# Performance work log

Measured on AMD Instinct MI355X. Metric: run time of the kernel, lower is better.

Reference implementation:

```python
import jax, jax.numpy as jnp
import numpy as np

D_MODEL = 1024


def setup_inputs() -> dict:
    key = jax.random.key(0)
    ks = jax.random.split(key, 9)
    B, S, D = 4, 2048, D_MODEL
    scale = 1.0 / np.sqrt(D)
    inp = {
        "tokens": jax.random.normal(ks[0], (B, S, D), dtype=jnp.float32),
        "Wq": jax.random.normal(ks[1], (D, D), dtype=jnp.float32) * scale,
        "bq": jnp.zeros((D,), dtype=jnp.float32),
        "Wk": jax.random.normal(ks[2], (D, D), dtype=jnp.float32) * scale,
        "bk": jnp.zeros((D,), dtype=jnp.float32),
        "Wv": jax.random.normal(ks[3], (D, D), dtype=jnp.float32) * scale,
        "bv": jnp.zeros((D,), dtype=jnp.float32),
        "Wo": jax.random.normal(ks[4], (D, D), dtype=jnp.float32) * scale,
        "bo": jnp.zeros((D,), dtype=jnp.float32),
    }
    return inp


def reference(tokens, Wq, bq, Wk, bk, Wv, bv, Wo, bo):
    # use_activation=True, use_residual=True
    residual = tokens
    x = jax.nn.gelu(tokens, approximate=False)  # F.gelu default is exact (erf)
    q = jnp.einsum("bsd,de->bse", x, Wq) + bq
    k = jnp.einsum("bsd,de->bse", x, Wk) + bk
    v = jnp.einsum("bsd,de->bse", x, Wv) + bv
    scale = 1.0 / jnp.sqrt(jnp.asarray(tokens.shape[-1], dtype=tokens.dtype))
    scores = jnp.einsum("bqd,bkd->bqk", q, k) * scale  # [B,S,S]
    attn = jax.nn.softmax(scores, axis=-1)
    mixed = jnp.einsum("bqk,bkd->bqd", attn, v)
    out = jnp.einsum("bsd,de->bse", mixed, Wo) + bo
    return out + residual
```

## Files before the change

### kernel.cpp

```cpp
#include <hip/hip_runtime.h>
#include <hip/hip_bf16.h>
#include <cstdint>
#include <cstddef>

typedef unsigned short u16;
using frag_ab = __attribute__((ext_vector_type(8))) short;
using f32x4   = __attribute__((ext_vector_type(4))) float;

__device__ __forceinline__ u16 f2bf(float x) {
    __hip_bfloat16 h = __float2bfloat16(x);
    return *reinterpret_cast<u16*>(&h);
}

__device__ __forceinline__ void gload_lds16(const u16* g, u16* l) {
    __builtin_amdgcn_global_load_lds(
        (const __attribute__((address_space(1))) uint32_t*)g,
        (__attribute__((address_space(3)))       uint32_t*)l,
        16, 0, 0);
}

#define WAITV4() do { asm volatile("s_waitcnt vmcnt(4)" ::: "memory"); \
                      __builtin_amdgcn_sched_barrier(0); } while (0)
#define WAITV0() do { asm volatile("s_waitcnt vmcnt(0)" ::: "memory"); \
                      __builtin_amdgcn_sched_barrier(0); } while (0)
#define BAR()    do { asm volatile("" ::: "memory"); __builtin_amdgcn_s_barrier(); \
                      __builtin_amdgcn_sched_barrier(0); } while (0)
#define LGKMC(N) do { asm volatile("s_waitcnt lgkmcnt(" #N ")" ::: "memory"); \
                      __builtin_amdgcn_sched_barrier(0); } while (0)
#define LGKM0()  LGKMC(0)

template<int EPI, int BN_>
__global__ __launch_bounds__(512, 2)
void gemm8p(const u16* __restrict__ A, const u16* __restrict__ Bt,
            void* __restrict__ C0,
            const float* __restrict__ b0, const float* __restrict__ resid,
            int K, int lda, int ldb, int ldc,
            long long sA, long long sB, long long sC, float alpha,
            float* __restrict__ partials)
{
    constexpr int NFQ    = BN_ / 64;
    constexpr int WN     = BN_ / 2;
    constexpr int BUFSTR = 16384 + BN_ * 64;
    __shared__ __align__(16) u16 lds[2 * BUFSTR];

    const int z = blockIdx.z;
    A  += (long long)z * sA;
    Bt += (long long)z * sB;

    const int gx  = gridDim.x;
    const int nwg = gx * gridDim.y;
    const int cpx = nwg >> 3;
    int lin = blockIdx.x + gx * blockIdx.y;
    lin = (lin & 7) * cpx + (lin >> 3);
    const int m0 = (lin / gx) * 256;
    const int n0 = (lin % gx) * BN_;

    const int t    = threadIdx.x;
    const int lane = t & 63;
    const int wave = t >> 6;
    const int wm   = wave >> 1;
    const int wn   = wave & 1;

    const int r0  = t >> 3;
    const int ssw = (t & 7) ^ (r0 & 7);
    const u16* gsA0_0 = A  + (size_t)(m0 +       r0) * lda + ssw * 8;
    const u16* gsA0_1 = A  + (size_t)(m0 +  64 + r0) * lda + ssw * 8;
    const u16* gsA1_0 = A  + (size_t)(m0 + 128 + r0) * lda + ssw * 8;
    const u16* gsA1_1 = A  + (size_t)(m0 + 192 + r0) * lda + ssw * 8;
    const u16* gsB0_0 = Bt + (size_t)(n0 +       r0) * ldb + ssw * 8;
    const u16* gsB0_1 = Bt + (size_t)(n0 +  64 + r0) * ldb + ssw * 8;
    const u16* gsB1_0 = (BN_ == 256) ? Bt + (size_t)(n0 + 128 + r0) * ldb + ssw * 8 : gsB0_0;
    const u16* gsB1_1 = (BN_ == 256) ? Bt + (size_t)(n0 + 192 + r0) * ldb + ssw * 8 : gsB0_1;

#define OPO_A 0
#define OPO_B 16384
#define STAGE(BI, OP, H, KT) do {                                              \
    gload_lds16(gs##OP##H##_0 + (size_t)(KT) * 64,                             \
                lds + (BI) * BUFSTR + OPO_##OP + (H) * 8192 + t * 8);          \
    gload_lds16(gs##OP##H##_1 + (size_t)(KT) * 64,                             \
                lds + (BI) * BUFSTR + OPO_##OP + (H) * 8192 + 4096 + t * 8);   \
} while (0)

    const int ar   = lane & 15;
    const int ko   = lane >> 4;
    const int aoff = (wm * 64 + ar) * 64;
    const int boff = OPO_B + (wn * WN + ar) * 64;
    const int as0  = ((0 + ko) ^ (ar & 7)) * 8;
    const int as1  = ((4 + ko) ^ (ar & 7)) * 8;

    frag_ab areg[2][2];
    frag_ab breg[2][NFQ][2];
    f32x4   acc[4][2 * NFQ] = {};

#define RDA(BI, MQ) do { _Pragma("unroll") for (int mf = 0; mf < 2; ++mf) {    \
    areg[mf][0] = *(const frag_ab*)(lds + (BI)*BUFSTR + aoff + ((MQ)*2+mf)*1024 + as0); \
    areg[mf][1] = *(const frag_ab*)(lds + (BI)*BUFSTR + aoff + ((MQ)*2+mf)*1024 + as1); } } while (0)

#define RDB(BI, NQ) do { _Pragma("unroll") for (int jf = 0; jf < NFQ; ++jf) {  \
    breg[NQ][jf][0] = *(const frag_ab*)(lds + (BI)*BUFSTR + boff + ((NQ)*NFQ+jf)*1024 + as0); \
    breg[NQ][jf][1] = *(const frag_ab*)(lds + (BI)*BUFSTR + boff + ((NQ)*NFQ+jf)*1024 + as1); } } while (0)

#define MMAQ(MQ, NQ) do { __builtin_amdgcn_s_setprio(1);                       \
    _Pragma("unroll") for (int mf = 0; mf < 2; ++mf)                           \
    _Pragma("unroll") for (int jf = 0; jf < NFQ; ++jf) {                       \
        acc[(MQ)*2+mf][(NQ)*NFQ+jf] = __builtin_amdgcn_mfma_f32_16x16x32_bf16( \
            areg[mf][0], breg[NQ][jf][0], acc[(MQ)*2+mf][(NQ)*NFQ+jf], 0,0,0); \
        acc[(MQ)*2+mf][(NQ)*NFQ+jf] = __builtin_amdgcn_mfma_f32_16x16x32_bf16( \
            areg[mf][1], breg[NQ][jf][1], acc[(MQ)*2+mf][(NQ)*NFQ+jf], 0,0,0); \
    } __builtin_amdgcn_s_setprio(0); } while (0)

    const int nk = K / 64;
    STAGE(0, A, 0, 0); STAGE(0, A, 1, 0); STAGE(0, B, 0, 0);
    if constexpr (BN_ == 256) STAGE(0, B, 1, 0);
    STAGE(1, B, 0, 1); STAGE(1, A, 0, 1);
    WAITV4();
    BAR();

    const int nIter = nk >> 1;
    for (int it = 0; it < nIter; ++it) {
        const int O  = 2 * it + 1;
        const int E2 = (2 * it + 2 < nk) ? 2 * it + 2 : nk - 1;
        const int O2 = (2 * it + 3 < nk) ? 2 * it + 3 : nk - 1;

        RDA(0, 0); RDB(0, 0);
        STAGE(1, A, 1, O);
        if constexpr (BN_ == 256) LGKMC(8);
        BAR(); LGKM0(); MMAQ(0, 0);
        RDB(0, 1);
        if constexpr (BN_ == 256) STAGE(1, B, 1, O);
        BAR(); LGKM0(); MMAQ(0, 1);
        RDA(0, 1);
        STAGE(0, B, 0, E2);
        BAR(); LGKM0(); MMAQ(1, 0);
        STAGE(0, A, 0, E2);
        WAITV4();
        BAR(); MMAQ(1, 1);
        RDA(1, 0); RDB(1, 0);
        STAGE(0, A, 1, E2);
        if constexpr (BN_ == 256) LGKMC(8);
        BAR(); LGKM0(); MMAQ(0, 0);
        RDB(1, 1);
        if constexpr (BN_ == 256) STAGE(0, B, 1, E2);
        BAR(); LGKM0(); MMAQ(0, 1);
        RDA(1, 1);
        STAGE(1, B, 0, O2);
        BAR(); LGKM0(); MMAQ(1, 0);
        STAGE(1, A, 0, O2);
        WAITV4();
        BAR(); MMAQ(1, 1);
    }

    const int cr = (lane >> 4) * 4;
    const int cc = lane & 15;

    float* fl = (float*)lds;
    if constexpr (EPI == 2) {
        WAITV0();
        BAR();
        if (t < 256) {
            const float* p = partials + ((size_t)z * 2048 + m0 + t) * 16;
            float s = 0.0f;
            #pragma unroll
            for (int i = 0; i < 16; ++i) s += p[i];
            fl[t] = 1.0f / s;
        }
        BAR();
    }

    float rs[4][4];
    if constexpr (EPI == 1) {
        #pragma unroll
        for (int mi = 0; mi < 4; ++mi)
            #pragma unroll
            for (int r = 0; r < 4; ++r) rs[mi][r] = 0.0f;
    }

    #pragma unroll
    for (int mi = 0; mi < 4; ++mi) {
        const int rowb = m0 + wm * 64 + mi * 16 + cr;
        const int rloc = wm * 64 + mi * 16 + cr;
        #pragma unroll
        for (int gj = 0; gj < 2 * NFQ; ++gj) {
            const int col = n0 + wn * WN + gj * 16 + cc;
            const float bvv = (EPI == 3) ? b0[col] : 0.0f;
            #pragma unroll
            for (int r = 0; r < 4; ++r) {
                const size_t row = (size_t)(rowb + r);
                float v = acc[mi][gj][r];
                if (EPI == 1) { v = __expf(v * alpha); rs[mi][r] += v; }
                if (EPI == 2) v *= fl[rloc + r];
                v += bvv;
                if (EPI == 3) {
                    v += resid[row * ldc + col];
                    ((float*)C0)[(size_t)z * sC + row * ldc + col] = v;
                } else {
                    ((u16*)C0)[(size_t)z * sC + row * ldc + col] = f2bf(v);
                }
            }
        }
    }

    if constexpr (EPI == 1) {
        #pragma unroll
        for (int mi = 0; mi < 4; ++mi)
            #pragma unroll
            for (int r = 0; r < 4; ++r) {
                float s = rs[mi][r];
                s += __shfl_xor(s, 1); s += __shfl_xor(s, 2);
                s += __shfl_xor(s, 4); s += __shfl_xor(s, 8);
                rs[mi][r] = s;
            }
        if (cc == 0) {
            const int chunk = (n0 >> 7) + wn;
            #pragma unroll
            for (int mi = 0; mi < 4; ++mi) {
                const int rowb = m0 + wm * 64 + mi * 16 + cr;
                #pragma unroll
                for (int r = 0; r < 4; ++r)
                    partials[((size_t)z * 2048 + rowb + r) * 16 + chunk] = rs[mi][r];
            }
        }
    }
#undef STAGE
#undef RDA
#undef RDB
#undef MMAQ
#undef OPO_A
#undef OPO_B
}

__global__ __launch_bounds__(256, 2)
void gemm128_qkv(const u16* __restrict__ A, const u16* __restrict__ Bt,
                 void* __restrict__ C0, void* __restrict__ C1, void* __restrict__ C2,
                 const float* __restrict__ b0, const float* __restrict__ b1,
                 const float* __restrict__ b2,
                 int K, int lda, int ldb, int ldc)
{
    constexpr int BUFSTR = 16384;
    __shared__ __align__(16) u16 lds[2 * BUFSTR];

    const int gx  = gridDim.x;
    const int nwg = gx * gridDim.y;
    const int cpx = nwg >> 3;
    int lin = blockIdx.x + gx * blockIdx.y;
    lin = (lin & 7) * cpx + (lin >> 3);
    const int m0 = (lin / gx) * 128;
    const int n0 = (lin % gx) * 128;

    const int t    = threadIdx.x;
    const int lane = t & 63;
    const int wave = t >> 6;
    const int wm   = wave >> 1;
    const int wn   = wave & 1;

    const int r0  = t >> 3;
    const int ssw = (t & 7) ^ (r0 & 7);
    const u16* gsA0_0 = A  + (size_t)(m0 +       r0) * lda + ssw * 8;
    const u16* gsA0_1 = A  + (size_t)(m0 +  32 + r0) * lda + ssw * 8;
    const u16* gsA1_0 = A  + (size_t)(m0 +  64 + r0) * lda + ssw * 8;
    const u16* gsA1_1 = A  + (size_t)(m0 +  96 + r0) * lda + ssw * 8;
    const u16* gsB0_0 = Bt + (size_t)(n0 +       r0) * ldb + ssw * 8;
    const u16* gsB0_1 = Bt + (size_t)(n0 +  32 + r0) * ldb + ssw * 8;
    const u16* gsB1_0 = Bt + (size_t)(n0 +  64 + r0) * ldb + ssw * 8;
    const u16* gsB1_1 = Bt + (size_t)(n0 +  96 + r0) * ldb + ssw * 8;

#define OPO_A 0
#define OPO_B 8192
#define STAGE(BI, OP, H, KT) do {                                              \
    gload_lds16(gs##OP##H##_0 + (size_t)(KT) * 64,                             \
                lds + (BI) * BUFSTR + OPO_##OP + (H) * 4096 + t * 8);          \
    gload_lds16(gs##OP##H##_1 + (size_t)(KT) * 64,                             \
                lds + (BI) * BUFSTR + OPO_##OP + (H) * 4096 + 2048 + t * 8);   \
} while (0)

    const int ar   = lane & 15;
    const int ko   = lane >> 4;
    const int aoff = (wm * 64 + ar) * 64;
    const int boff = OPO_B + (wn * 64 + ar) * 64;
    const int as0  = ((0 + ko) ^ (ar & 7)) * 8;
    const int as1  = ((4 + ko) ^ (ar & 7)) * 8;

    frag_ab areg[2][2];
    frag_ab breg[2][2][2];
    f32x4   acc[4][4] = {};

#define RDA(BI, MQ) do { _Pragma("unroll") for (int mf = 0; mf < 2; ++mf) {    \
    areg[mf][0] = *(const frag_ab*)(lds + (BI)*BUFSTR + aoff + ((MQ)*2+mf)*1024 + as0); \
    areg[mf][1] = *(const frag_ab*)(lds + (BI)*BUFSTR + aoff + ((MQ)*2+mf)*1024 + as1); } } while (0)

#define RDB(BI, NQ) do { _Pragma("unroll") for (int jf = 0; jf < 2; ++jf) {    \
    breg[NQ][jf][0] = *(const frag_ab*)(lds + (BI)*BUFSTR + boff + ((NQ)*2+jf)*1024 + as0); \
    breg[NQ][jf][1] = *(const frag_ab*)(lds + (BI)*BUFSTR + boff + ((NQ)*2+jf)*1024 + as1); } } while (0)

#define MMAQ(MQ, NQ) do { __builtin_amdgcn_s_setprio(1);                       \
    _Pragma("unroll") for (int mf = 0; mf < 2; ++mf)                           \
    _Pragma("unroll") for (int jf = 0; jf < 2; ++jf) {                         \
        acc[(MQ)*2+mf][(NQ)*2+jf] = __builtin_amdgcn_mfma_f32_16x16x32_bf16(   \
            areg[mf][0], breg[NQ][jf][0], acc[(MQ)*2+mf][(NQ)*2+jf], 0,0,0);   \
        acc[(MQ)*2+mf][(NQ)*2+jf] = __builtin_amdgcn_mfma_f32_16x16x32_bf16(   \
            areg[mf][1], breg[NQ][jf][1], acc[(MQ)*2+mf][(NQ)*2+jf], 0,0,0);   \
    } __builtin_amdgcn_s_setprio(0); } while (0)

    const int nk = K / 64;
    STAGE(0, A, 0, 0); STAGE(0, A, 1, 0); STAGE(0, B, 0, 0); STAGE(0, B, 1, 0);
    STAGE(1, B, 0, 1); STAGE(1, A, 0, 1);
    WAITV4();
    BAR();

    const int nIter = nk >> 1;
    for (int it = 0; it < nIter; ++it) {
        const int O  = 2 * it + 1;
        const int E2 = (2 * it + 2 < nk) ? 2 * it + 2 : nk - 1;
        const int O2 = (2 * it + 3 < nk) ? 2 * it + 3 : nk - 1;

        RDA(0, 0); RDB(0, 0); STAGE(1, A, 1, O);  BAR(); LGKM0(); MMAQ(0, 0);
        RDB(0, 1);            STAGE(1, B, 1, O);  BAR(); LGKM0(); MMAQ(0, 1);
        RDA(0, 1);            STAGE(0, B, 0, E2); BAR(); LGKM0(); MMAQ(1, 0);
        STAGE(0, A, 0, E2);   WAITV4();           BAR();          MMAQ(1, 1);
        RDA(1, 0); RDB(1, 0); STAGE(0, A, 1, E2); BAR(); LGKM0(); MMAQ(0, 0);
        RDB(1, 1);            STAGE(0, B, 1, E2); BAR(); LGKM0(); MMAQ(0, 1);
        RDA(1, 1);            STAGE(1, B, 0, O2); BAR(); LGKM0(); MMAQ(1, 0);
        STAGE(1, A, 0, O2);   WAITV4();           BAR();          MMAQ(1, 1);
    }

    const int cr = (lane >> 4) * 4;
    const int cc = lane & 15;

    const int plane = n0 >> 10;
    const int nc    = n0 & 1023;

    if (plane == 2) {
        WAITV0();
        BAR();
        constexpr int TP = 136;
        u16* T = lds;
        #pragma unroll
        for (int mi = 0; mi < 4; ++mi) {
            const int rloc = wm * 64 + mi * 16 + cr;
            #pragma unroll
            for (int gj = 0; gj < 4; ++gj) {
                const int cl = wn * 64 + gj * 16 + cc;
                const float bvv = b2[nc + cl];
                #pragma unroll
                for (int r = 0; r < 4; ++r)
                    T[cl * TP + rloc + r] = f2bf(acc[mi][gj][r] + bvv);
            }
        }
        BAR();
        const int bb   = m0 >> 11;
        const int s0   = m0 & 2047;
        const int d    = t >> 1;
        const int half = t & 1;
        const u16* src = T + d * TP + half * 64;
        u16* dg = (u16*)C2 + (size_t)bb * 1024 * 2048
                + (size_t)(nc + d) * 2048 + s0 + half * 64;
        #pragma unroll
        for (int j = 0; j < 8; ++j)
            ((uint4*)dg)[j] = ((const uint4*)src)[j];
    } else {
        void*        Cw = (plane == 0) ? C0 : C1;
        const float* bw = (plane == 0) ? b0 : b1;
        #pragma unroll
        for (int mi = 0; mi < 4; ++mi) {
            const int rowb = m0 + wm * 64 + mi * 16 + cr;
            #pragma unroll
            for (int gj = 0; gj < 4; ++gj) {
                const int col = nc + wn * 64 + gj * 16 + cc;
                const float bvv = bw[col];
                #pragma unroll
                for (int r = 0; r < 4; ++r) {
                    const size_t row = (size_t)(rowb + r);
                    ((u16*)Cw)[row * ldc + col] = f2bf(acc[mi][gj][r] + bvv);
                }
            }
        }
    }
#undef STAGE
#undef RDA
#undef RDB
#undef MMAQ
#undef OPO_A
#undef OPO_B
}

__global__ __launch_bounds__(256)
void prep_kernel(const float4* __restrict__ in, uint2* __restrict__ outp,
                 const float* __restrict__ W0, const float* __restrict__ W1,
                 const float* __restrict__ W2, const float* __restrict__ W3,
                 u16* __restrict__ WT, int D, int NG)
{
    __shared__ float tile[32][33];
    const int b = blockIdx.x;
    const int t = threadIdx.x;
    if (b < NG) {
        const int i = b * 256 + t;
        float4 x = in[i];
        auto g = [](float v) { return 0.5f * v * (1.0f + erff(v * 0.70710678118654752f)); };
        union { u16 u[4]; uint2 q; } pk;
        pk.u[0] = f2bf(g(x.x));
        pk.u[1] = f2bf(g(x.y));
        pk.u[2] = f2bf(g(x.z));
        pk.u[3] = f2bf(g(x.w));
        outp[i] = pk.q;
        return;
    }
    const int j   = b - NG;
    const int z   = j >> 10;
    const int rem = j & 1023;
    const int n0  = (rem & 31) * 32;
    const int k0  = (rem >> 5) * 32;
    const float* W = (z == 0) ? W0 : (z == 1) ? W1 : (z == 2) ? W2 : W3;
    u16* o = WT + (size_t)z * D * D;
    const int tx = t & 31, ty = t >> 5;
    #pragma unroll
    for (int r = 0; r < 4; ++r)
        tile[ty + 8 * r][tx] = W[(size_t)(k0 + ty + 8 * r) * D + n0 + tx];
    __syncthreads();
    #pragma unroll
    for (int r = 0; r < 4; ++r)
        o[(size_t)(n0 + ty + 8 * r) * D + k0 + tx] = f2bf(tile[tx][ty + 8 * r]);
}

extern "C" void kernel_launch(void* const* d_in, const int* in_sizes, int n_in,
                              void* d_out, int out_size, void* d_ws, size_t ws_size,
                              hipStream_t stream)
{
    const int B = 4, S = 2048, D = 1024;
    const int M = B * S;

    const float* tokens = (const float*)d_in[0];
    const float* Wq = (const float*)d_in[1];
    const float* bq = (const float*)d_in[2];
    const float* Wk = (const float*)d_in[3];
    const float* bk = (const float*)d_in[4];
    const float* Wv = (const float*)d_in[5];
    const float* bv = (const float*)d_in[6];
    const float* Wo = (const float*)d_in[7];
    const float* bo = (const float*)d_in[8];
    float* out = (float*)d_out;

    char* ws = (char*)d_ws;
    size_t o = 0;
    u16* x_bf = (u16*)(ws + o); o += (size_t)M * D * 2;
    u16* wT   = (u16*)(ws + o); o += (size_t)4 * D * D * 2;
    u16* q_bf = (u16*)(ws + o); o += (size_t)M * D * 2;
    u16* k_bf = (u16*)(ws + o); o += (size_t)M * D * 2;
    u16* vt   = (u16*)(ws + o); o += (size_t)M * D * 2;
    u16*   E        = (u16*)(ws + o);   o += (size_t)B * S * S * 2;
    float* partials = (float*)(ws + o); o += (size_t)B * S * 16 * 4;
    u16* mixed = x_bf;

    const int NG = M * D / 4 / 256;
    prep_kernel<<<dim3(NG + 4096), dim3(256), 0, stream>>>(
        (const float4*)tokens, (uint2*)x_bf, Wq, Wk, Wv, Wo, wT, D, NG);

    gemm128_qkv<<<dim3(3 * D / 128, M / 128, 1), dim3(256), 0, stream>>>(
        x_bf, wT, q_bf, k_bf, vt, bq, bk, bv, D, D, D, D);

    gemm8p<1, 256><<<dim3(S / 256, S / 256, B), dim3(512), 0, stream>>>(
        q_bf, k_bf, E, nullptr, nullptr,
        D, D, D, S, (long long)S * D, (long long)S * D, (long long)S * S, 0.03125f,
        partials);

    gemm8p<2, 128><<<dim3(D / 128, S / 256, B), dim3(512), 0, stream>>>(
        E, vt, mixed, nullptr, nullptr,
        S, S, S, D, (long long)S * S, (long long)D * S, (long long)S * D, 1.0f,
        partials);

    gemm8p<3, 128><<<dim3(D / 128, M / 256, 1), dim3(512), 0, stream>>>(
        mixed, wT + 3 * D * D, out, bo, tokens,
        D, D, D, D, 0, 0, 0, 1.0f, nullptr);
}
```

Before: 172.7 us.

## Split QKV projection into 256-tile QK GEMM and separate V-transpose GEMM

Replaces the single 128x128-tile fused QKV GEMM with a new 512-thread 256x256-tile kernel for Q and K, using a triple-buffered A / double-buffered B LDS pipeline, plus a dedicated 128-tile kernel for V with its transposed store. The larger tiles raise arithmetic intensity and cut global traffic for the Q/K projection. The V epilogue now packs four bf16 values into one LDS store, and the GELU prep kernel processes eight elements per thread. The cost is an extra kernel launch, a very large LDS footprint and high register pressure in the 256-tile kernel, which may limit occupancy.

```diff
diff --git a/kernel.cpp b/kernel.cpp
--- a/kernel.cpp
+++ b/kernel.cpp
@@ -229,12 +229,139 @@
 #undef OPO_B
 }
 
+__global__ __launch_bounds__(512, 2)
+void gemmQK3(const u16* __restrict__ A, const u16* __restrict__ Bt,
+             u16* __restrict__ C0, const float* __restrict__ b0,
+             const float* __restrict__ b1,
+             int K, int lda, int ldb, int ldc, long long sC)
+{
+    __shared__ __align__(16) u16 lds[81920];
+
+    const int gx  = gridDim.x;
+    const int nwg = gx * gridDim.y;
+    const int cpx = nwg >> 3;
+    int lin = blockIdx.x + gx * blockIdx.y;
+    lin = (lin & 7) * cpx + (lin >> 3);
+    const int m0 = (lin / gx) * 256;
+    const int n0 = (lin % gx) * 256;
+
+    const int t    = threadIdx.x;
+    const int lane = t & 63;
+    const int wave = t >> 6;
+    const int wm   = wave >> 1;
+    const int wn   = wave & 1;
+
+    const int r0  = t >> 3;
+    const int ssw = (t & 7) ^ (r0 & 7);
+    const u16* gsA_0 = A  + (size_t)(m0 +       r0) * lda + ssw * 8;
+    const u16* gsA_1 = A  + (size_t)(m0 +  64 + r0) * lda + ssw * 8;
+    const u16* gsA_2 = A  + (size_t)(m0 + 128 + r0) * lda + ssw * 8;
+    const u16* gsA_3 = A  + (size_t)(m0 + 192 + r0) * lda + ssw * 8;
+    const u16* gsB_0 = Bt + (size_t)(n0 +       r0) * ldb + ssw * 8;
+    const u16* gsB_1 = Bt + (size_t)(n0 +  64 + r0) * ldb + ssw * 8;
+    const u16* gsB_2 = Bt + (size_t)(n0 + 128 + r0) * ldb + ssw * 8;
+    const u16* gsB_3 = Bt + (size_t)(n0 + 192 + r0) * ldb + ssw * 8;
+
+#define STA(BUF, H, KT) do {                                                   \
+    gload_lds16(((H) ? gsA_2 : gsA_0) + (size_t)(KT) * 64,                     \
+                lds + (BUF) * 16384 + (H) * 8192 + t * 8);                     \
+    gload_lds16(((H) ? gsA_3 : gsA_1) + (size_t)(KT) * 64,                     \
+                lds + (BUF) * 16384 + (H) * 8192 + 4096 + t * 8);              \
+} while (0)
+#define STB(BUF, H, KT) do {                                                   \
+    gload_lds16(((H) ? gsB_2 : gsB_0) + (size_t)(KT) * 64,                     \
+                lds + 49152 + (BUF) * 16384 + (H) * 8192 + t * 8);             \
+    gload_lds16(((H) ? gsB_3 : gsB_1) + (size_t)(KT) * 64,                     \
+                lds + 49152 + (BUF) * 16384 + (H) * 8192 + 4096 + t * 8);      \
+} while (0)
+
+    const int ar   = lane & 15;
+    const int ko   = lane >> 4;
+    const int aoff = (wm * 64 + ar) * 64;
+    const int boff = 49152 + (wn * 128 + ar) * 64;
+    const int as0  = ((0 + ko) ^ (ar & 7)) * 8;
+    const int as1  = ((4 + ko) ^ (ar & 7)) * 8;
+
+    frag_ab areg[2][2];
+    frag_ab breg[2][4][2];
+    f32x4   acc[4][8] = {};
+
+#define RDA3(AB, MQ) do { _Pragma("unroll") for (int mf = 0; mf < 2; ++mf) {   \
+    areg[mf][0] = *(const frag_ab*)(lds + (AB) + aoff + ((MQ)*2+mf)*1024 + as0); \
+    areg[mf][1] = *(const frag_ab*)(lds + (AB) + aoff + ((MQ)*2+mf)*1024 + as1); } } while (0)
+
+#define RDB3(BB, NQ) do { _Pragma("unroll") for (int jf = 0; jf < 4; ++jf) {   \
+    breg[NQ][jf][0] = *(const frag_ab*)(lds + (BB) + boff + ((NQ)*4+jf)*1024 + as0); \
+    breg[NQ][jf][1] = *(const frag_ab*)(lds + (BB) + boff + ((NQ)*4+jf)*1024 + as1); } } while (0)
+
+#define MMAQ3(MQ, NQ) do { __builtin_amdgcn_s_setprio(1);                      \
+    _Pragma("unroll") for (int mf = 0; mf < 2; ++mf)                           \
+    _Pragma("unroll") for (int jf = 0; jf < 4; ++jf) {                         \
+        acc[(MQ)*2+mf][(NQ)*4+jf] = __builtin_amdgcn_mfma_f32_16x16x32_bf16(   \
+            areg[mf][0], breg[NQ][jf][0], acc[(MQ)*2+mf][(NQ)*4+jf], 0,0,0);   \
+        acc[(MQ)*2+mf][(NQ)*4+jf] = __builtin_amdgcn_mfma_f32_16x16x32_bf16(   \
+            areg[mf][1], breg[NQ][jf][1], acc[(MQ)*2+mf][(NQ)*4+jf], 0,0,0);   \
+    } __builtin_amdgcn_s_setprio(0); } while (0)
+
+    const int nk = K / 64;
+    STA(0, 0, 0); STA(0, 1, 0);
+    STB(0, 0, 0); STB(0, 1, 0);
+    STA(1, 0, 1); STA(1, 1, 1);
+    WAITV4();
+    BAR();
+
+    int ab = 0, bb = 0;
+    for (int tt = 0; tt < nk; ++tt) {
+        const int ab2 = (ab + 2 >= 3) ? ab - 1 : ab + 2;
+        const int bb1 = bb ^ 1;
+        const int tB  = (tt + 1 < nk) ? tt + 1 : nk - 1;
+        const int tA  = (tt + 2 < nk) ? tt + 2 : nk - 1;
+        const int AB = ab * 16384, BB = bb * 16384;
+        RDA3(AB, 0); RDB3(BB, 0);
+        STB(bb1, 0, tB);
+        LGKMC(8);
+        BAR(); LGKM0(); MMAQ3(0, 0);
+        RDB3(BB, 1);
+        STB(bb1, 1, tB);
+        BAR(); LGKM0(); MMAQ3(0, 1);
+        RDA3(AB, 1);
+        STA(ab2, 0, tA);
+        BAR(); LGKM0(); MMAQ3(1, 0);
+        STA(ab2, 1, tA);
+        WAITV4();
+        BAR(); MMAQ3(1, 1);
+        ab = (ab + 1 >= 3) ? 0 : ab + 1;
+        bb = bb1;
+    }
+
+    const int cr = (lane >> 4) * 4;
+    const int cc = lane & 15;
+    #pragma unroll
+    for (int mi = 0; mi < 4; ++mi) {
+        const int rowb = m0 + wm * 64 + mi * 16 + cr;
+        #pragma unroll
+        for (int gj = 0; gj < 8; ++gj) {
+            const int col = n0 + wn * 128 + gj * 16 + cc;
+            const int plane = col >> 10;
+            const int cl    = col & 1023;
+            const float bvv = ((plane == 0) ? b0 : b1)[cl];
+            u16* Cw = C0 + (size_t)plane * sC;
+            #pragma unroll
+            for (int r = 0; r < 4; ++r)
+                Cw[(size_t)(rowb + r) * ldc + cl] = f2bf(acc[mi][gj][r] + bvv);
+        }
+    }
+#undef STA
+#undef STB
+#undef RDA3
+#undef RDB3
+#undef MMAQ3
+}
+
 __global__ __launch_bounds__(256, 2)
-void gemm128_qkv(const u16* __restrict__ A, const u16* __restrict__ Bt,
-                 void* __restrict__ C0, void* __restrict__ C1, void* __restrict__ C2,
-                 const float* __restrict__ b0, const float* __restrict__ b1,
-                 const float* __restrict__ b2,
-                 int K, int lda, int ldb, int ldc)
+void gemm128_v(const u16* __restrict__ A, const u16* __restrict__ Bt,
+               u16* __restrict__ VT, const float* __restrict__ bv,
+               int K, int lda, int ldb)
 {
     constexpr int BUFSTR = 16384;
     __shared__ __align__(16) u16 lds[2 * BUFSTR];
@@ -326,55 +453,33 @@
     const int cr = (lane >> 4) * 4;
     const int cc = lane & 15;
 
-    const int plane = n0 >> 10;
-    const int nc    = n0 & 1023;
-
-    if (plane == 2) {
-        WAITV0();
-        BAR();
-        constexpr int TP = 136;
-        u16* T = lds;
+    WAITV0();
+    BAR();
+    constexpr int TP = 136;
+    u16* T = lds;
+    #pragma unroll
+    for (int mi = 0; mi < 4; ++mi) {
+        const int rloc = wm * 64 + mi * 16 + cr;
         #pragma unroll
-        for (int mi = 0; mi < 4; ++mi) {
-            const int rloc = wm * 64 + mi * 16 + cr;
-            #pragma unroll
-            for (int gj = 0; gj < 4; ++gj) {
-                const int cl = wn * 64 + gj * 16 + cc;
-                const float bvv = b2[nc + cl];
-                #pragma unroll
-                for (int r = 0; r < 4; ++r)
-                    T[cl * TP + rloc + r] = f2bf(acc[mi][gj][r] + bvv);
-            }
+        for (int gj = 0; gj < 4; ++gj) {
+            const int cl = wn * 64 + gj * 16 + cc;
+            const float bvv = bv[n0 + cl];
+            union { u16 u[4]; uint2 q; } pk;
+            #pragma unroll
+            for (int r = 0; r < 4; ++r) pk.u[r] = f2bf(acc[mi][gj][r] + bvv);
+            *(uint2*)&T[cl * TP + rloc] = pk.q;
         }
-        BAR();
-        const int bb   = m0 >> 11;
-        const int s0   = m0 & 2047;
-        const int d    = t >> 1;
-        const int half = t & 1;
-        const u16* src = T + d * TP + half * 64;
-        u16* dg = (u16*)C2 + (size_t)bb * 1024 * 2048
-                + (size_t)(nc + d) * 2048 + s0 + half * 64;
-        #pragma unroll
-        for (int j = 0; j < 8; ++j)
-            ((uint4*)dg)[j] = ((const uint4*)src)[j];
-    } else {
-        void*        Cw = (plane == 0) ? C0 : C1;
-        const float* bw = (plane == 0) ? b0 : b1;
-        #pragma unroll
-        for (int mi = 0; mi < 4; ++mi) {
-            const int rowb = m0 + wm * 64 + mi * 16 + cr;
-            #pragma unroll
-            for (int gj = 0; gj < 4; ++gj) {
-                const int col = nc + wn * 64 + gj * 16 + cc;
-                const float bvv = bw[col];
-                #pragma unroll
-                for (int r = 0; r < 4; ++r) {
-                    const size_t row = (size_t)(rowb + r);
-                    ((u16*)Cw)[row * ldc + col] = f2bf(acc[mi][gj][r] + bvv);
-                }
-            }
-        }
-    }
+    }
+    BAR();
+    const int bb   = m0 >> 11;
+    const int s0   = m0 & 2047;
+    const int d    = t >> 1;
+    const int half = t & 1;
+    const u16* src = T + d * TP + half * 64;
+    u16* dg = VT + (size_t)bb * 1024 * 2048 + (size_t)(n0 + d) * 2048 + s0 + half * 64;
+    #pragma unroll
+    for (int j = 0; j < 8; ++j)
+        ((uint4*)dg)[j] = ((const uint4*)src)[j];
 #undef STAGE
 #undef RDA
 #undef RDB
@@ -384,7 +489,7 @@
 }
 
 __global__ __launch_bounds__(256)
-void prep_kernel(const float4* __restrict__ in, uint2* __restrict__ outp,
+void prep_kernel(const float4* __restrict__ in, uint4* __restrict__ outp,
                  const float* __restrict__ W0, const float* __restrict__ W1,
                  const float* __restrict__ W2, const float* __restrict__ W3,
                  u16* __restrict__ WT, int D, int NG)
@@ -393,15 +498,15 @@
     const int b = blockIdx.x;
     const int t = threadIdx.x;
     if (b < NG) {
-        const int i = b * 256 + t;
-        float4 x = in[i];
+        const int i = (b * 256 + t) * 2;
+        float4 x0 = in[i], x1 = in[i + 1];
         auto g = [](float v) { return 0.5f * v * (1.0f + erff(v * 0.70710678118654752f)); };
-        union { u16 u[4]; uint2 q; } pk;
-        pk.u[0] = f2bf(g(x.x));
-        pk.u[1] = f2bf(g(x.y));
-        pk.u[2] = f2bf(g(x.z));
-        pk.u[3] = f2bf(g(x.w));
-        outp[i] = pk.q;
+        union { u16 u[8]; uint4 q; } pk;
+        pk.u[0] = f2bf(g(x0.x)); pk.u[1] = f2bf(g(x0.y));
+        pk.u[2] = f2bf(g(x0.z)); pk.u[3] = f2bf(g(x0.w));
+        pk.u[4] = f2bf(g(x1.x)); pk.u[5] = f2bf(g(x1.y));
+        pk.u[6] = f2bf(g(x1.z)); pk.u[7] = f2bf(g(x1.w));
+        outp[b * 256 + t] = pk.q;
         return;
     }
     const int j   = b - NG;
@@ -450,12 +555,15 @@
     float* partials = (float*)(ws + o); o += (size_t)B * S * 16 * 4;
     u16* mixed = x_bf;
 
-    const int NG = M * D / 4 / 256;
+    const int NG = M * D / 8 / 256;
     prep_kernel<<<dim3(NG + 4096), dim3(256), 0, stream>>>(
-        (const float4*)tokens, (uint2*)x_bf, Wq, Wk, Wv, Wo, wT, D, NG);
-
-    gemm128_qkv<<<dim3(3 * D / 128, M / 128, 1), dim3(256), 0, stream>>>(
-        x_bf, wT, q_bf, k_bf, vt, bq, bk, bv, D, D, D, D);
+        (const float4*)tokens, (uint4*)x_bf, Wq, Wk, Wv, Wo, wT, D, NG);
+
+    gemmQK3<<<dim3(2 * D / 256, M / 256, 1), dim3(512), 0, stream>>>(
+        x_bf, wT, q_bf, bq, bk, D, D, D, D, (long long)M * D);
+
+    gemm128_v<<<dim3(D / 128, M / 128, 1), dim3(256), 0, stream>>>(
+        x_bf, wT + 2 * D * D, vt, bv, D, D, D);
 
     gemm8p<1, 256><<<dim3(S / 256, S / 256, B), dim3(512), 0, stream>>>(
         q_bf, k_bf, E, nullptr, nullptr,
```

Measured after the change: 168.3 us. 2.6% less time.
